# Kernel tuning notes

Hardware: AMD Instinct MI355X
Metric: run time of the kernel (lower is better)

## Reference

```python
import jax, jax.numpy as jnp
import numpy as np

B, N, D = 2, 2048, 768
H = 12
HD = D // H  # 64

def setup_inputs() -> dict:
    key = jax.random.key(0)
    ks = jax.random.split(key, 5)
    scale = 1.0 / np.sqrt(D)
    return {
        "x": jax.random.normal(ks[0], (B, N, D), dtype=jnp.float32),
        "W_kqv": jax.random.normal(ks[1], (H, 3 * HD, D), dtype=jnp.float32) * scale,
        "b_kqv": jax.random.normal(ks[2], (H, 3 * HD), dtype=jnp.float32) * 0.01,
        "W_proj": jax.random.normal(ks[3], (D, D), dtype=jnp.float32) * scale,
        "b_proj": jax.random.normal(ks[4], (D,), dtype=jnp.float32) * 0.01,
    }

def reference(x, W_kqv, b_kqv, W_proj, b_proj):
    # Per-head Linear: x @ W_h^T + b_h, all heads at once -> [B, H, N, 3*HD]
    kqv = jnp.einsum('bnd,hod->bhno', x, W_kqv) + b_kqv[None, :, None, :]
    k, q, v = jnp.split(kqv, 3, axis=-1)  # each [B, H, N, HD]
    # scores = q @ k^T / sqrt(head_dim)  (attention_scores(a=k, b=q))
    scores = jnp.einsum('bhqd,bhkd->bhqk', q, k) / jnp.sqrt(jnp.asarray(HD, x.dtype))
    # causal mask (tril): masked_fill with -inf where mask == 0
    causal = jnp.tril(jnp.ones((N, N), dtype=bool))
    scores = jnp.where(causal[None, None, :, :], scores, -jnp.inf)
    attn = jax.nn.softmax(scores, axis=-1)
    sa = jnp.einsum('bhqk,bhkd->bhqd', attn, v)  # [B, H, N, HD]
    # concat heads along feature dim (head order preserved)
    sa = sa.transpose(0, 2, 1, 3).reshape(B, N, D)
    # output projection
    return sa @ W_proj.T + b_proj
```

## Files before the change

### kernel.cpp

```cpp
#include <hip/hip_runtime.h>

#define BB 2
#define SEQ 2048
#define DIM 768
#define NH 12
#define HD 64

typedef _Float16 half8 __attribute__((ext_vector_type(8)));
typedef float floatx4 __attribute__((ext_vector_type(4)));

__device__ __forceinline__ void gl_lds16(const _Float16* g, _Float16* l) {
    __builtin_amdgcn_global_load_lds(
        (const __attribute__((address_space(1))) void*)g,
        (__attribute__((address_space(3))) void*)l, 16, 0, 0);
}

__global__ __launch_bounds__(256)
void cvt3(const float* __restrict__ s0, _Float16* __restrict__ d0, int nb0,
          const float* __restrict__ s1, _Float16* __restrict__ d1, int nb1,
          const float* __restrict__ s2, _Float16* __restrict__ d2) {
    int b = blockIdx.x;
    const float* s; _Float16* d;
    if (b < nb0)            { s = s0; d = d0; }
    else if (b < nb0 + nb1) { s = s1; d = d1; b -= nb0; }
    else                    { s = s2; d = d2; b -= nb0 + nb1; }
    const int i = (b * 256 + threadIdx.x) * 8;
    float4 a = *(const float4*)(s + i);
    float4 c = *(const float4*)(s + i + 4);
    half8 h;
    h[0] = (_Float16)a.x; h[1] = (_Float16)a.y; h[2] = (_Float16)a.z; h[3] = (_Float16)a.w;
    h[4] = (_Float16)c.x; h[5] = (_Float16)c.y; h[6] = (_Float16)c.z; h[7] = (_Float16)c.w;
    *(half8*)(d + i) = h;
}

#define GEMM_CORE(APTR, BPTR)                                                   \
    __shared__ _Float16 Asl[2][128 * 32];                                       \
    __shared__ _Float16 Bsl[2][128 * 32];                                       \
    const int t = threadIdx.x, w = t >> 6, lane = t & 63;                       \
    const int quad = lane >> 4, l15 = lane & 15;                                \
    const int wm = w >> 1, wn = w & 1;                                          \
    const int m0 = blockIdx.y * 128, c0 = blockIdx.x * 128;                     \
    const floatx4 z4 = {0.f, 0.f, 0.f, 0.f};                                    \
    floatx4 acc[4][4];                                                          \
    _Pragma("unroll") for (int i = 0; i < 4; ++i)                               \
        _Pragma("unroll") for (int j = 0; j < 4; ++j) acc[i][j] = z4;           \
    const _Float16* pA = APTR + (size_t)(m0 + w * 32 + l15) * DIM + quad * 8;   \
    const _Float16* pB = BPTR + (size_t)(c0 + w * 32 + l15) * DIM + quad * 8;   \
    gl_lds16(pA,            &Asl[0][(w * 2 + 0) * 512]);                        \
    gl_lds16(pA + 16 * DIM, &Asl[0][(w * 2 + 1) * 512]);                        \
    gl_lds16(pB,            &Bsl[0][(w * 2 + 0) * 512]);                        \
    gl_lds16(pB + 16 * DIM, &Bsl[0][(w * 2 + 1) * 512]);                        \
    for (int k0 = 0, it = 0; k0 < DIM; k0 += 32, ++it) {                        \
        const int buf = it & 1;                                                 \
        __syncthreads();                                                        \
        if (k0 + 32 < DIM) {                                                    \
            gl_lds16(pA + k0 + 32,            &Asl[buf ^ 1][(w * 2 + 0) * 512]);\
            gl_lds16(pA + k0 + 32 + 16 * DIM, &Asl[buf ^ 1][(w * 2 + 1) * 512]);\
            gl_lds16(pB + k0 + 32,            &Bsl[buf ^ 1][(w * 2 + 0) * 512]);\
            gl_lds16(pB + k0 + 32 + 16 * DIM, &Bsl[buf ^ 1][(w * 2 + 1) * 512]);\
        }                                                                       \
        half8 af[4], bf[4];                                                     \
        _Pragma("unroll") for (int i = 0; i < 4; ++i)                           \
            af[i] = *(const half8*)&Asl[buf][(wm * 4 + i) * 512 + lane * 8];    \
        _Pragma("unroll") for (int j = 0; j < 4; ++j)                           \
            bf[j] = *(const half8*)&Bsl[buf][(wn * 4 + j) * 512 + lane * 8];    \
        _Pragma("unroll") for (int i = 0; i < 4; ++i)                           \
            _Pragma("unroll") for (int j = 0; j < 4; ++j)                       \
                acc[i][j] = __builtin_amdgcn_mfma_f32_16x16x32_f16(             \
                    af[i], bf[j], acc[i][j], 0, 0, 0);                          \
    }

__global__ __launch_bounds__(256)
void kqv_gemm2(const _Float16* __restrict__ xh, const _Float16* __restrict__ Wh,
               const float* __restrict__ bias, _Float16* __restrict__ kb,
               _Float16* __restrict__ qb, _Float16* __restrict__ vb) {
    GEMM_CORE(xh, Wh)
    #pragma unroll
    for (int j = 0; j < 4; ++j) {
        const int cbase = c0 + (wn * 4 + j) * 16;
        const int h = cbase / 192;
        const int rem = cbase - h * 192;
        const int part = rem >> 6;
        const int d = (rem & 63) + l15;
        _Float16* dst = (part == 0) ? kb : (part == 1 ? qb : vb);
        const float bv = bias[cbase + l15];
        #pragma unroll
        for (int i = 0; i < 4; ++i)
            #pragma unroll
            for (int r = 0; r < 4; ++r) {
                const int m = m0 + (wm * 4 + i) * 16 + quad * 4 + r;
                const int bidx = m >> 11, n = m & (SEQ - 1);
                dst[(((size_t)(bidx * NH + h) * SEQ + n) << 6) + d] =
                    (_Float16)(acc[i][j][r] + bv);
            }
    }
}

__global__ __launch_bounds__(256)
void proj_gemm2(const _Float16* __restrict__ A, const _Float16* __restrict__ Wh,
                const float* __restrict__ bias, float* __restrict__ out) {
    GEMM_CORE(A, Wh)
    #pragma unroll
    for (int j = 0; j < 4; ++j) {
        const int cbase = c0 + (wn * 4 + j) * 16;
        const float bv = bias[cbase + l15];
        #pragma unroll
        for (int i = 0; i < 4; ++i)
            #pragma unroll
            for (int r = 0; r < 4; ++r) {
                const int m = m0 + (wm * 4 + i) * 16 + quad * 4 + r;
                out[(size_t)m * DIM + cbase + l15] = acc[i][j][r] + bv;
            }
    }
}

__global__ __launch_bounds__(256)
void v_transpose(const _Float16* __restrict__ vb, _Float16* __restrict__ vbT) {
    __shared__ _Float16 T[64 * 72];
    const int t = threadIdx.x;
    const int s0 = blockIdx.x * 64;
    const size_t base = (size_t)blockIdx.y * (SEQ * HD);
    {
        const int s = t >> 2, doff = (t & 3) * 16;
        const _Float16* src = vb + base + (size_t)(s0 + s) * HD + doff;
        *(half8*)&T[s * 72 + doff]     = *(const half8*)src;
        *(half8*)&T[s * 72 + doff + 8] = *(const half8*)(src + 8);
    }
    __syncthreads();
    {
        const int d = t >> 2, soff = (t & 3) * 16;
        half8 o0, o1;
        #pragma unroll
        for (int k = 0; k < 8; ++k) o0[k] = T[(soff + k) * 72 + d];
        #pragma unroll
        for (int k = 0; k < 8; ++k) o1[k] = T[(soff + 8 + k) * 72 + d];
        _Float16* dst = vbT + base + (size_t)d * SEQ + s0 + soff;
        *(half8*)dst       = o0;
        *(half8*)(dst + 8) = o1;
    }
}

__global__ __launch_bounds__(256)
void attn_mfma(const _Float16* __restrict__ qb, const _Float16* __restrict__ kbuf,
               const _Float16* __restrict__ vbT, _Float16* __restrict__ sa,
               _Float16* __restrict__ Opart, float* __restrict__ lpart) {
    __shared__ _Float16 Kl[2][64 * 64];
    __shared__ _Float16 Vl[2][64 * 64];
    __shared__ _Float16 Pl[4][16 * 64];
    int u = blockIdx.x, qt, p, np;
    if (u < 8)       { qt = u;                            p = 0;      np = 1; }
    else if (u < 24) { int v = u - 8;  qt = 8  + (v >> 1); p = v & 1; np = 2; }
    else if (u < 48) { int v = u - 24; qt = 16 + v / 3;    p = v % 3; np = 3; }
    else             { int v = u - 48; qt = 24 + (v >> 2); p = v & 3; np = 4; }
    const int kt0 = p * 8;
    const int ktn = (p == np - 1) ? (qt - kt0 + 1) : 8;

    const int bh = blockIdx.y;
    const int t = threadIdx.x, w = t >> 6, lane = t & 63, quad = lane >> 4, l15 = lane & 15;
    const size_t base = (size_t)bh * (SEQ * HD);
    const int i0 = qt * 64 + w * 16;
    _Float16* Pw = Pl[w];
    const _Float16* Kg = kbuf + base;
    const _Float16* Vg = vbT + base;

    const int lr = lane >> 3, gg = lane & 7;
    const int gs = (gg ^ (lr & 7)) * 8;

    half8 aq[2];
    aq[0] = *(const half8*)(qb + base + (size_t)(i0 + l15) * HD + quad * 8);
    aq[1] = *(const half8*)(qb + base + (size_t)(i0 + l15) * HD + 32 + quad * 8);
    const _Float16 qs = (_Float16)(0.125f * 1.44269504f);
    #pragma unroll
    for (int k = 0; k < 8; ++k) { aq[0][k] *= qs; aq[1][k] *= qs; }

    const floatx4 z4 = {0.f, 0.f, 0.f, 0.f};
    floatx4 O[4];
    #pragma unroll
    for (int dt = 0; dt < 4; ++dt) O[dt] = z4;
    float l_part[4] = {0.f, 0.f, 0.f, 0.f};

    #pragma unroll
    for (int pp = 0; pp < 2; ++pp) {
        const int c = w * 2 + pp, row = c * 8 + lr;
        gl_lds16(Kg + (size_t)(kt0 * 64 + row) * HD + gs,  &Kl[0][c * 512]);
        gl_lds16(Vg + (size_t)row * SEQ + kt0 * 64 + gs,   &Vl[0][c * 512]);
    }

    const int swz = l15 & 7;
    const int prow = quad * 4;

    for (int it = 0; it < ktn; ++it) {
        const int kt = kt0 + it;
        const int buf = it & 1;
        const int j0 = kt * 64;
        __syncthreads();

        if (it + 1 < ktn) {
            const _Float16* Kn = Kg + (size_t)(j0 + 64) * HD;
            const _Float16* Vn = Vg + (j0 + 64);
            #pragma unroll
            for (int pp = 0; pp < 2; ++pp) {
                const int c = w * 2 + pp, row = c * 8 + lr;
                gl_lds16(Kn + (size_t)row * HD + gs,  &Kl[buf ^ 1][c * 512]);
                gl_lds16(Vn + (size_t)row * SEQ + gs, &Vl[buf ^ 1][c * 512]);
            }
        }

        floatx4 S[4];
        #pragma unroll
        for (int nt = 0; nt < 4; ++nt) S[nt] = z4;
        #pragma unroll
        for (int ks = 0; ks < 2; ++ks)
            #pragma unroll
            for (int nt = 0; nt < 4; ++nt) {
                half8 bk = *(const half8*)&Kl[buf][(nt * 16 + l15) * 64 +
                                                   (((ks * 4 + quad) ^ swz) << 3)];
                S[nt] = __builtin_amdgcn_mfma_f32_16x16x32_f16(aq[ks], bk, S[nt], 0, 0, 0);
            }

        asm volatile("" ::: "memory");
        if (kt == qt) {
            #pragma unroll
            for (int nt = 0; nt < 4; ++nt) {
                const int j = j0 + nt * 16 + l15;
                #pragma unroll
                for (int r = 0; r < 4; ++r) {
                    float pv = exp2f(S[nt][r]);
                    if (j > (i0 + prow + r)) pv = 0.f;
                    l_part[r] += pv;
                    const int row = prow + r, col = nt * 16 + l15;
                    Pw[row * 64 + ((((col >> 3) ^ (row & 7))) << 3) + (col & 7)] = (_Float16)pv;
                }
            }
        } else {
            #pragma unroll
            for (int nt = 0; nt < 4; ++nt) {
                #pragma unroll
                for (int r = 0; r < 4; ++r) {
                    float pv = exp2f(S[nt][r]);
                    l_part[r] += pv;
                    const int row = prow + r, col = nt * 16 + l15;
                    Pw[row * 64 + ((((col >> 3) ^ (row & 7))) << 3) + (col & 7)] = (_Float16)pv;
                }
            }
        }
        asm volatile("" ::: "memory");
        #pragma unroll
        for (int ks = 0; ks < 2; ++ks) {
            half8 ap = *(const half8*)&Pw[l15 * 64 + (((ks * 4 + quad) ^ swz) << 3)];
            #pragma unroll
            for (int dt = 0; dt < 4; ++dt) {
                half8 bv = *(const half8*)&Vl[buf][(dt * 16 + l15) * 64 +
                                                    (((ks * 4 + quad) ^ swz) << 3)];
                O[dt] = __builtin_amdgcn_mfma_f32_16x16x32_f16(ap, bv, O[dt], 0, 0, 0);
            }
        }
    }

    if (np == 1) {
        const int bidx = bh / NH, h = bh - bidx * NH;
        #pragma unroll
        for (int r = 0; r < 4; ++r) {
            float rs = l_part[r];
            #pragma unroll
            for (int off = 1; off < 16; off <<= 1) rs += __shfl_xor(rs, off);
            const float inv = 1.0f / rs;
            const int i = i0 + quad * 4 + r;
            #pragma unroll
            for (int dt = 0; dt < 4; ++dt)
                sa[(size_t)(bidx * SEQ + i) * DIM + h * HD + dt * 16 + l15] =
                    (_Float16)(O[dt][r] * inv);
        }
    } else {
        const size_t slot = ((size_t)(bh * 32 + qt) * 4 + p);
        _Float16* Od = Opart + slot * 4096;
        float*    ld = lpart + slot * 64;
        #pragma unroll
        for (int r = 0; r < 4; ++r) {
            float rs = l_part[r];
            #pragma unroll
            for (int off = 1; off < 16; off <<= 1) rs += __shfl_xor(rs, off);
            const int row = w * 16 + quad * 4 + r;
            ld[row] = rs;
            #pragma unroll
            for (int dt = 0; dt < 4; ++dt)
                Od[row * 64 + dt * 16 + l15] = (_Float16)O[dt][r];
        }
    }
}

__global__ __launch_bounds__(256)
void attn_combine(const _Float16* __restrict__ Opart, const float* __restrict__ lpart,
                  _Float16* __restrict__ sa) {
    const int qt = 8 + blockIdx.x;
    const int bh = blockIdx.y;
    const int np = (qt >> 3) + 1;
    const int t = threadIdx.x;
    const int row = t >> 2, d0 = (t & 3) * 16;
    const size_t slot0 = ((size_t)(bh * 32 + qt) * 4);

    float lsum = 0.f;
    for (int p = 0; p < np; ++p) lsum += lpart[(slot0 + p) * 64 + row];

    float acc[16];
    #pragma unroll
    for (int k = 0; k < 16; ++k) acc[k] = 0.f;
    for (int p = 0; p < np; ++p) {
        const _Float16* src = Opart + (slot0 + p) * 4096 + row * 64 + d0;
        half8 a = *(const half8*)src;
        half8 b = *(const half8*)(src + 8);
        #pragma unroll
        for (int k = 0; k < 8; ++k) { acc[k] += (float)a[k]; acc[8 + k] += (float)b[k]; }
    }
    const float inv = 1.0f / lsum;
    const int bidx = bh / NH, h = bh - bidx * NH;
    _Float16* dst = sa + (size_t)(bidx * SEQ + qt * 64 + row) * DIM + h * HD + d0;
    half8 o0, o1;
    #pragma unroll
    for (int k = 0; k < 8; ++k) { o0[k] = (_Float16)(acc[k] * inv); o1[k] = (_Float16)(acc[8 + k] * inv); }
    *(half8*)dst       = o0;
    *(half8*)(dst + 8) = o1;
}

extern "C" void kernel_launch(void* const* d_in, const int* in_sizes, int n_in,
                              void* d_out, int out_size, void* d_ws, size_t ws_size,
                              hipStream_t stream) {
    (void)in_sizes; (void)n_in; (void)out_size; (void)ws_size;
    const float* x  = (const float*)d_in[0];
    const float* Wk = (const float*)d_in[1];
    const float* bk = (const float*)d_in[2];
    const float* Wp = (const float*)d_in[3];
    const float* bp = (const float*)d_in[4];
    float* out = (float*)d_out;

    _Float16* ws = (_Float16*)d_ws;
    const size_t per = (size_t)BB * NH * SEQ * HD;
    const int nx = BB * SEQ * DIM;
    const int nwk = NH * 3 * HD * DIM;
    const int nwp = DIM * DIM;
    _Float16* kb  = ws;
    _Float16* qb  = ws + per;
    _Float16* vb  = ws + 2 * per;
    _Float16* vbT = ws + 3 * per;
    _Float16* sa  = ws + 4 * per;
    _Float16* xh  = ws + 5 * per;
    _Float16* Wkh = xh + nx;
    _Float16* Wph = Wkh + nwk;
    _Float16* Opart = Wph + nwp;
    float*    lpart = (float*)(Opart + (size_t)24 * 32 * 4 * 4096);

    const int nb0 = nx / 2048, nb1 = nwk / 2048, nb2 = nwp / 2048;
    cvt3<<<dim3(nb0 + nb1 + nb2), 256, 0, stream>>>(x, xh, nb0, Wk, Wkh, nb1, Wp, Wph);

    kqv_gemm2  <<<dim3(18, 32), 256, 0, stream>>>(xh, Wkh, bk, kb, qb, vb);
    v_transpose<<<dim3(32, 24), 256, 0, stream>>>(vb, vbT);
    attn_mfma  <<<dim3(80, 24), 256, 0, stream>>>(qb, kb, vbT, sa, Opart, lpart);
    attn_combine<<<dim3(24, 24), 256, 0, stream>>>(Opart, lpart, sa);
    proj_gemm2 <<<dim3(6, 32), 256, 0, stream>>>(sa, Wph, bp, out);
}
```

Measured before the change: 185.4 us.

## Transpose QK^T MFMA output so each lane packs P rows with vector stores

Swaps the MFMA operand order in the score computation so each lane holds four consecutive key columns for one query row. P tiles can then be packed with cvt_pkrtz and written as 4-wide half vectors instead of scalar stores, and the row-sum reduction collapses to a single per-lane accumulator with two cross-quad shuffles. The causal mask is recomputed in the transposed index space, the P swizzle is changed to match, and s_setprio is raised around the MFMA blocks. The new swizzle and mask indexing carry a correctness risk, and round-toward-zero conversion slightly changes numerics.

```diff
diff --git a/kernel.cpp b/kernel.cpp
--- a/kernel.cpp
+++ b/kernel.cpp
@@ -7,12 +7,21 @@
 #define HD 64
 
 typedef _Float16 half8 __attribute__((ext_vector_type(8)));
+typedef _Float16 h4v __attribute__((ext_vector_type(4)));
+typedef __fp16 f16x2 __attribute__((ext_vector_type(2)));
 typedef float floatx4 __attribute__((ext_vector_type(4)));
 
 __device__ __forceinline__ void gl_lds16(const _Float16* g, _Float16* l) {
     __builtin_amdgcn_global_load_lds(
         (const __attribute__((address_space(1))) void*)g,
         (__attribute__((address_space(3))) void*)l, 16, 0, 0);
+}
+
+__device__ __forceinline__ h4v pack4(float a, float b, float c, float d) {
+    union { f16x2 h2[2]; h4v h4; } u;
+    u.h2[0] = __builtin_amdgcn_cvt_pkrtz(a, b);
+    u.h2[1] = __builtin_amdgcn_cvt_pkrtz(c, d);
+    return u.h4;
 }
 
 __global__ __launch_bounds__(256)
@@ -177,7 +186,7 @@
     floatx4 O[4];
     #pragma unroll
     for (int dt = 0; dt < 4; ++dt) O[dt] = z4;
-    float l_part[4] = {0.f, 0.f, 0.f, 0.f};
+    float l_one = 0.f;
 
     #pragma unroll
     for (int pp = 0; pp < 2; ++pp) {
@@ -187,7 +196,8 @@
     }
 
     const int swz = l15 & 7;
-    const int prow = quad * 4;
+    const int sswz = (l15 & 7) << 1;
+    const int srow = l15 * 64;
 
     for (int it = 0; it < ktn; ++it) {
         const int kt = kt0 + it;
@@ -209,45 +219,52 @@
         floatx4 S[4];
         #pragma unroll
         for (int nt = 0; nt < 4; ++nt) S[nt] = z4;
+        __builtin_amdgcn_s_setprio(1);
         #pragma unroll
         for (int ks = 0; ks < 2; ++ks)
             #pragma unroll
             for (int nt = 0; nt < 4; ++nt) {
                 half8 bk = *(const half8*)&Kl[buf][(nt * 16 + l15) * 64 +
                                                    (((ks * 4 + quad) ^ swz) << 3)];
-                S[nt] = __builtin_amdgcn_mfma_f32_16x16x32_f16(aq[ks], bk, S[nt], 0, 0, 0);
-            }
+                S[nt] = __builtin_amdgcn_mfma_f32_16x16x32_f16(bk, aq[ks], S[nt], 0, 0, 0);
+            }
+        __builtin_amdgcn_s_setprio(0);
 
         asm volatile("" ::: "memory");
         if (kt == qt) {
             #pragma unroll
             for (int nt = 0; nt < 4; ++nt) {
-                const int j = j0 + nt * 16 + l15;
+                float pv[4];
                 #pragma unroll
                 for (int r = 0; r < 4; ++r) {
-                    float pv = exp2f(S[nt][r]);
-                    if (j > (i0 + prow + r)) pv = 0.f;
-                    l_part[r] += pv;
-                    const int row = prow + r, col = nt * 16 + l15;
-                    Pw[row * 64 + ((((col >> 3) ^ (row & 7))) << 3) + (col & 7)] = (_Float16)pv;
+                    float pvv = exp2f(S[nt][r]);
+                    if (nt * 16 + quad * 4 + r > w * 16 + l15) pvv = 0.f;
+                    l_one += pvv;
+                    pv[r] = pvv;
                 }
+                *(h4v*)&Pw[srow + (((nt * 4 + quad) ^ sswz) << 2)] =
+                    pack4(pv[0], pv[1], pv[2], pv[3]);
             }
         } else {
             #pragma unroll
             for (int nt = 0; nt < 4; ++nt) {
+                float pv[4];
                 #pragma unroll
                 for (int r = 0; r < 4; ++r) {
-                    float pv = exp2f(S[nt][r]);
-                    l_part[r] += pv;
-                    const int row = prow + r, col = nt * 16 + l15;
-                    Pw[row * 64 + ((((col >> 3) ^ (row & 7))) << 3) + (col & 7)] = (_Float16)pv;
+                    float pvv = exp2f(S[nt][r]);
+                    l_one += pvv;
+                    pv[r] = pvv;
                 }
+                *(h4v*)&Pw[srow + (((nt * 4 + quad) ^ sswz) << 2)] =
+                    pack4(pv[0], pv[1], pv[2], pv[3]);
             }
         }
         asm volatile("" ::: "memory");
+
+        __builtin_amdgcn_s_setprio(1);
         #pragma unroll
         for (int ks = 0; ks < 2; ++ks) {
-            half8 ap = *(const half8*)&Pw[l15 * 64 + (((ks * 4 + quad) ^ swz) << 3)];
+            half8 ap = *(const half8*)&Pw[srow + (((((ks * 4 + quad) << 1)) ^ sswz) << 2)];
             #pragma unroll
             for (int dt = 0; dt < 4; ++dt) {
                 half8 bv = *(const half8*)&Vl[buf][(dt * 16 + l15) * 64 +
@@ -255,33 +272,33 @@
                 O[dt] = __builtin_amdgcn_mfma_f32_16x16x32_f16(ap, bv, O[dt], 0, 0, 0);
             }
         }
-    }
+        __builtin_amdgcn_s_setprio(0);
+    }
+
+    float rs = l_one;
+    rs += __shfl_xor(rs, 16);
+    rs += __shfl_xor(rs, 32);
 
     if (np == 1) {
+        const float inv = 1.0f / rs;
         const int bidx = bh / NH, h = bh - bidx * NH;
         #pragma unroll
         for (int r = 0; r < 4; ++r) {
-            float rs = l_part[r];
-            #pragma unroll
-            for (int off = 1; off < 16; off <<= 1) rs += __shfl_xor(rs, off);
-            const float inv = 1.0f / rs;
+            const float invr = __shfl(inv, quad * 4 + r);
             const int i = i0 + quad * 4 + r;
             #pragma unroll
             for (int dt = 0; dt < 4; ++dt)
                 sa[(size_t)(bidx * SEQ + i) * DIM + h * HD + dt * 16 + l15] =
-                    (_Float16)(O[dt][r] * inv);
+                    (_Float16)(O[dt][r] * invr);
         }
     } else {
         const size_t slot = ((size_t)(bh * 32 + qt) * 4 + p);
         _Float16* Od = Opart + slot * 4096;
         float*    ld = lpart + slot * 64;
+        if (lane < 16) ld[w * 16 + lane] = rs;
         #pragma unroll
         for (int r = 0; r < 4; ++r) {
-            float rs = l_part[r];
-            #pragma unroll
-            for (int off = 1; off < 16; off <<= 1) rs += __shfl_xor(rs, off);
             const int row = w * 16 + quad * 4 + r;
-            ld[row] = rs;
             #pragma unroll
             for (int dt = 0; dt < 4; ++dt)
                 Od[row * 64 + dt * 16 + l15] = (_Float16)O[dt][r];
```

Result: no change. 183.5 us (-1.0%).
